# Kernel optimization log

Hardware: AMD Instinct MI355X
Metric: run time of the kernel (lower is better)

The kernel has to match this reference:

```python
import jax, jax.numpy as jnp
import numpy as np
from jax import lax

EPS = 1e-7   # keras.backend.epsilon()
NEG = -1e30  # log-space -inf surrogate


def setup_inputs() -> dict:
    key = jax.random.key(0)
    k1, k2 = jax.random.split(key)
    B, T, C, L = 512, 1024, 256, 64
    logits = jax.random.uniform(k1, (B, T, C), dtype=jnp.float32)
    y_pred = logits / jnp.sum(logits, axis=-1, keepdims=True)  # valid probability rows
    y_true = jax.random.randint(k2, (B, L), 0, C - 1, dtype=jnp.int32)  # avoid blank=C-1
    return {"y_true": y_true, "y_pred": y_pred}


def _ctc_loss(y_pred, y_true):
    # y_pred: [B,T,C] probabilities; y_true: [B,L] labels; blank = C-1,
    # input_length = T and label_length = L for all batch elements (as in the module).
    B, T, C = y_pred.shape
    L = y_true.shape[1]
    S = 2 * L + 1
    blank = C - 1
    lp = jnp.log(y_pred + EPS)  # [B,T,C]

    # extended label sequence: blank, l1, blank, l2, ..., blank  -> [B,S]
    ext = jnp.full((B, S), blank, dtype=jnp.int32).at[:, 1::2].set(y_true.astype(jnp.int32))
    # per-step emission log-probs gathered on the extended sequence: [T,B,S]
    lp_ext = jnp.take_along_axis(lp, ext[:, None, :], axis=2).transpose(1, 0, 2)

    # skip transition (s-2 -> s) allowed iff ext[s] != blank and ext[s] != ext[s-2]
    ext_sm2 = jnp.pad(ext, ((0, 0), (2, 0)), constant_values=blank)[:, :S]
    allow_skip = (ext != blank) & (ext != ext_sm2)  # [B,S]

    alpha0 = jnp.full((B, S), NEG, dtype=lp.dtype)
    alpha0 = alpha0.at[:, 0].set(lp_ext[0, :, 0]).at[:, 1].set(lp_ext[0, :, 1])

    def step(alpha, lp_t):
        a1 = alpha
        a2 = jnp.pad(alpha, ((0, 0), (1, 0)), constant_values=NEG)[:, :S]
        a3 = jnp.where(allow_skip,
                       jnp.pad(alpha, ((0, 0), (2, 0)), constant_values=NEG)[:, :S],
                       NEG)
        m = jnp.maximum(jnp.maximum(a1, a2), a3)
        new = m + jnp.log(jnp.exp(a1 - m) + jnp.exp(a2 - m) + jnp.exp(a3 - m)) + lp_t
        return new, None

    alpha, _ = lax.scan(step, alpha0, lp_ext[1:])
    # sequence ends on final blank or final label
    total = jnp.logaddexp(alpha[:, S - 1], alpha[:, S - 2])
    return -total[:, None]  # [B,1], matching expand_dims in ctc_batch_cost


def reference(y_true, y_pred):
    return _ctc_loss(y_pred, y_true)
```

## Files before the change

### kernel.cpp

```cpp
#include <hip/hip_runtime.h>
#include <stdint.h>


#define EPS 1e-7f
#define NEG -1e30f

constexpr int Bb = 512;
constexpr int Tt = 1024;
constexpr int Cc = 256;
constexpr int Ll = 64;
constexpr int BLANK = Cc - 1;
constexpr int CH = 32;
constexpr int NCH = Tt / CH;

__device__ __forceinline__ void dma_row(const float* __restrict__ g,
                                        float* l) {
    __builtin_amdgcn_global_load_lds(
        (const __attribute__((address_space(1))) void*)g,
        (__attribute__((address_space(3))) void*)l, 16, 0, 0);
}

__global__ __launch_bounds__(64, 1) void ctc_fwd_kernel(
    const int* __restrict__ y_true,
    const float* __restrict__ y_pred,
    float* __restrict__ out)
{
    const int b = blockIdx.x;
    const int lane = threadIdx.x;

    const float* __restrict__ row0 = y_pred + (size_t)b * Tt * Cc;

    __shared__ float ring[2 * CH * Cc];

    const int lab = y_true[b * Ll + lane];
    const int lab_prev = __shfl_up(lab, 1);
    const bool allow = (lane == 0) ? true : (lab != lab_prev);

    for (int r = 0; r < CH; ++r)
        dma_row(row0 + r * Cc + lane * 4, &ring[r * Cc]);
    for (int r = 0; r < CH; ++r)
        dma_row(row0 + (CH + r) * Cc + lane * 4, &ring[(CH + r) * Cc]);

    asm volatile("s_waitcnt vmcnt(32)" ::: "memory");

    float ae, ao, a128;
    {
        const float pl0 = ring[lab];
        const float pb0 = ring[BLANK];
        ae = (lane == 0) ? __logf(pb0 + EPS) : NEG;
        ao = (lane == 0) ? __logf(pl0 + EPS) : NEG;
        a128 = NEG;
    }

    auto update = [&](float gl, float gb) {
        const float lpl = __logf(gl + EPS);
        const float lpb = __logf(gb + EPS);
        float ao_up = __shfl_up(ao, 1);
        if (lane == 0) ao_up = NEG;

        const float m2 = fmaxf(ae, ao_up);
        const float ne =
            m2 + __logf(__expf(ae - m2) + __expf(ao_up - m2)) + lpb;

        const float a3 = allow ? ao_up : NEG;
        const float m3 = fmaxf(fmaxf(ao, ae), a3);
        const float no =
            m3 +
            __logf(__expf(ao - m3) + __expf(ae - m3) + __expf(a3 - m3)) +
            lpl;

        const float m1 = fmaxf(a128, ao);
        const float n128 =
            m1 + __logf(__expf(a128 - m1) + __expf(ao - m1)) + lpb;

        ae = ne;
        ao = no;
        a128 = n128;
    };

#pragma unroll
    for (int r = 1; r < CH; ++r)
        update(ring[r * Cc + lab], ring[r * Cc + BLANK]);

    for (int c = 1; c < NCH; ++c) {
        const float* buf = &ring[(c & 1) * CH * Cc];
        float* nbuf = &ring[((c + 1) & 1) * CH * Cc];
        if (c + 1 < NCH) {
            const float* src = row0 + (size_t)(c + 1) * CH * Cc;
            for (int r = 0; r < CH; ++r)
                dma_row(src + r * Cc + lane * 4, nbuf + r * Cc);
            asm volatile("s_waitcnt vmcnt(32)" ::: "memory");
        } else {
            asm volatile("s_waitcnt vmcnt(0)" ::: "memory");
        }
#pragma unroll
        for (int r = 0; r < CH; ++r)
            update(buf[r * Cc + lab], buf[r * Cc + BLANK]);
    }

    if (lane == 63) {
        const float m = fmaxf(a128, ao);
        out[b] = -(m + __logf(__expf(a128 - m) + __expf(ao - m)));
    }
}

extern "C" void kernel_launch(void* const* d_in, const int* in_sizes, int n_in,
                              void* d_out, int out_size, void* d_ws,
                              size_t ws_size, hipStream_t stream) {
    const int* y_true = (const int*)d_in[0];
    const float* y_pred = (const float*)d_in[1];
    float* out = (float*)d_out;

    ctc_fwd_kernel<<<dim3(Bb), dim3(64), 0, stream>>>(y_true, y_pred, out);
}
```

Baseline: 809.0 us.

## Gather only needed emission probabilities into registers instead of DMAing full rows

Replaces the LDS ring buffer, which pulled whole 256-class rows into shared memory through global_load_lds, with direct per-lane gathers of only the label and blank probabilities into double-buffered register arrays. The chunk size is halved to keep register pressure manageable. This cuts global traffic from full rows to two scattered floats per lane per timestep and removes the LDS round trip. In exchange the loads are uncoalesced, the blank load is redundant across all lanes, and latency hiding now depends on the compiler scheduling the register prefetch ahead of the serial recurrence.

```diff
diff --git a/kernel.cpp b/kernel.cpp
--- a/kernel.cpp
+++ b/kernel.cpp
@@ -10,15 +10,8 @@
 constexpr int Cc = 256;
 constexpr int Ll = 64;
 constexpr int BLANK = Cc - 1;
-constexpr int CH = 32;
+constexpr int CH = 16;
 constexpr int NCH = Tt / CH;
-
-__device__ __forceinline__ void dma_row(const float* __restrict__ g,
-                                        float* l) {
-    __builtin_amdgcn_global_load_lds(
-        (const __attribute__((address_space(1))) void*)g,
-        (__attribute__((address_space(3))) void*)l, 16, 0, 0);
-}
 
 __global__ __launch_bounds__(64, 1) void ctc_fwd_kernel(
     const int* __restrict__ y_true,
@@ -30,27 +23,25 @@
 
     const float* __restrict__ row0 = y_pred + (size_t)b * Tt * Cc;
 
-    __shared__ float ring[2 * CH * Cc];
-
     const int lab = y_true[b * Ll + lane];
     const int lab_prev = __shfl_up(lab, 1);
     const bool allow = (lane == 0) ? true : (lab != lab_prev);
 
-    for (int r = 0; r < CH; ++r)
-        dma_row(row0 + r * Cc + lane * 4, &ring[r * Cc]);
-    for (int r = 0; r < CH; ++r)
-        dma_row(row0 + (CH + r) * Cc + lane * 4, &ring[(CH + r) * Cc]);
+    float glA[CH], gbA[CH], glB[CH], gbB[CH];
 
-    asm volatile("s_waitcnt vmcnt(32)" ::: "memory");
+#define LOAD_CHUNK(GL, GB, K)                                   \
+    _Pragma("unroll") for (int r = 0; r < CH; ++r) {            \
+        const int t = (K) * CH + r;                             \
+        GL[r] = row0[t * Cc + lab];                             \
+        GB[r] = row0[t * Cc + BLANK];                           \
+    }
 
-    float ae, ao, a128;
-    {
-        const float pl0 = ring[lab];
-        const float pb0 = ring[BLANK];
-        ae = (lane == 0) ? __logf(pb0 + EPS) : NEG;
-        ao = (lane == 0) ? __logf(pl0 + EPS) : NEG;
-        a128 = NEG;
-    }
+    LOAD_CHUNK(glA, gbA, 0)
+    LOAD_CHUNK(glB, gbB, 1)
+
+    float ae = (lane == 0) ? __logf(gbA[0] + EPS) : NEG;
+    float ao = (lane == 0) ? __logf(glA[0] + EPS) : NEG;
+    float a128 = NEG;
 
     auto update = [&](float gl, float gb) {
         const float lpl = __logf(gl + EPS);
@@ -79,24 +70,18 @@
     };
 
 #pragma unroll
-    for (int r = 1; r < CH; ++r)
-        update(ring[r * Cc + lab], ring[r * Cc + BLANK]);
+    for (int r = 1; r < CH; ++r) update(glA[r], gbA[r]);
 
-    for (int c = 1; c < NCH; ++c) {
-        const float* buf = &ring[(c & 1) * CH * Cc];
-        float* nbuf = &ring[((c + 1) & 1) * CH * Cc];
-        if (c + 1 < NCH) {
-            const float* src = row0 + (size_t)(c + 1) * CH * Cc;
-            for (int r = 0; r < CH; ++r)
-                dma_row(src + r * Cc + lane * 4, nbuf + r * Cc);
-            asm volatile("s_waitcnt vmcnt(32)" ::: "memory");
-        } else {
-            asm volatile("s_waitcnt vmcnt(0)" ::: "memory");
-        }
+    for (int k = 1; k + 1 < NCH; k += 2) {
+        LOAD_CHUNK(glA, gbA, k + 1)
 #pragma unroll
-        for (int r = 0; r < CH; ++r)
-            update(buf[r * Cc + lab], buf[r * Cc + BLANK]);
+        for (int r = 0; r < CH; ++r) update(glB[r], gbB[r]);
+        LOAD_CHUNK(glB, gbB, k + 2)
+#pragma unroll
+        for (int r = 0; r < CH; ++r) update(glA[r], gbA[r]);
     }
+#pragma unroll
+    for (int r = 0; r < CH; ++r) update(glB[r], gbB[r]);
 
     if (lane == 63) {
         const float m = fmaxf(a128, ao);
```

Result: slower. 858.0 us (+6.1%).
